# Performance work log

Measured on AMD Instinct MI355X. Metric: run time of the kernel, lower is better.

Reference implementation:

```python
import jax, jax.numpy as jnp
import numpy as np

N_HEADS = 4
D_K = 32
C = 128
SCALE = D_K ** (-0.5)


def setup_inputs() -> dict:
    key = jax.random.key(0)
    k1, k2, k3, k4, k5 = jax.random.split(key, 5)
    x = jax.random.normal(k1, (16, C, 32, 32), dtype=jnp.float32)
    # nn.Linear(C, n_heads*d_k*3): weight [out, in], bias [out]
    Wp = jax.random.normal(k2, (N_HEADS * D_K * 3, C), dtype=jnp.float32) * (C ** -0.5)
    bp = jax.random.normal(k3, (N_HEADS * D_K * 3,), dtype=jnp.float32) * 0.01
    # nn.Linear(n_heads*d_k, C)
    Wo = jax.random.normal(k4, (C, N_HEADS * D_K), dtype=jnp.float32) * ((N_HEADS * D_K) ** -0.5)
    bo = jax.random.normal(k5, (C,), dtype=jnp.float32) * 0.01
    return {"x": x, "Wp": Wp, "bp": bp, "Wo": Wo, "bo": bo}


def reference(x, Wp, bp, Wo, bo):
    b, c, h, w = x.shape
    n = h * w
    # (b,c,h,w) -> (b, n, c); NOTE: GroupNorm from __init__ is never applied in forward.
    xf = x.reshape(b, c, n).transpose(0, 2, 1)
    qkv = (xf @ Wp.T + bp).reshape(b, n, N_HEADS, 3 * D_K)
    q, k, v = jnp.split(qkv, 3, axis=-1)  # each (b, n, heads, d_k)
    attn = jnp.einsum('bihd,bjhd->bijh', q, k) * SCALE  # (b, n, n, heads)
    # Faithful to original: softmax over LAST axis = heads axis (original code bug)
    attn = jax.nn.softmax(attn, axis=-1)
    res = jnp.einsum('bijh,bjhd->bihd', attn, v).reshape(b, n, N_HEADS * D_K)
    res = res @ Wo.T + bo + xf
    return res.transpose(0, 2, 1).reshape(b, c, h, w)
```

## Files before the change

kernel.cpp:

```cpp
#include <hip/hip_runtime.h>

typedef short s8v __attribute__((ext_vector_type(8)));
typedef float f4v __attribute__((ext_vector_type(4)));

#define NTOK 1024
#define CD 128
#define QSCALE 0.25506953149031838f

__device__ __forceinline__ ushort f2bf(float x) {
    union { float f; unsigned u; } v; v.f = x;
    unsigned u = v.u + 0x7fff + ((v.u >> 16) & 1);
    return (ushort)(u >> 16);
}
__device__ __forceinline__ float bf2f(ushort x) {
    union { unsigned u; float f; } v; v.u = ((unsigned)x) << 16;
    return v.f;
}
__device__ __forceinline__ void gl_lds16(const ushort* g, ushort* l) {
    __builtin_amdgcn_global_load_lds(
        (const __attribute__((address_space(1))) unsigned int*)(g),
        (__attribute__((address_space(3))) unsigned int*)(l), 16, 0, 0);
}
__device__ __forceinline__ unsigned cvt_pk_bf16(float lo, float hi) {
    unsigned r;
    asm("v_cvt_pk_bf16_f32 %0, %1, %2" : "=v"(r) : "v"(lo), "v"(hi));
    return r;
}

__global__ __launch_bounds__(256) void k_pre(const float* __restrict__ x,
                                             const float* __restrict__ Wp,
                                             const float* __restrict__ Wo,
                                             ushort* __restrict__ xt,
                                             ushort* __restrict__ wpre) {
    const int t = threadIdx.x;
    const int bx = blockIdx.x;
    if (bx < 256) {
        __shared__ ushort tile[128 * 68];
        const int b = bx >> 4;
        const int n0 = (bx & 15) << 6;
        #pragma unroll
        for (int p = 0; p < 8; ++p) {
            const int c = p * 16 + (t >> 4);
            const int n4 = t & 15;
            const float4 v = *(const float4*)&x[(b * CD + c) * NTOK + n0 + n4 * 4];
            ushort4 o;
            o.x = f2bf(v.x); o.y = f2bf(v.y); o.z = f2bf(v.z); o.w = f2bf(v.w);
            *(ushort4*)&tile[c * 68 + n4 * 4] = o;
        }
        __syncthreads();
        #pragma unroll
        for (int p = 0; p < 4; ++p) {
            const int nl = t >> 2;
            const int g = (t & 3) + p * 4;
            s8v tmp;
            #pragma unroll
            for (int e = 0; e < 8; ++e) tmp[e] = (short)tile[(g * 8 + e) * 68 + nl];
            const int n = n0 + nl;
            *(s8v*)&xt[(b * NTOK + n) * CD + ((g ^ (nl & 7)) * 8)] = tmp;
        }
    } else {
        const int kind = bx - 256;
        ushort* dst = wpre + kind * (CD * CD);
        for (int e = t * 4; e < CD * CD; e += 1024) {
            const int f = e >> 7, c = e & 127;
            const float* src;
            if (kind == 3) src = &Wo[f * CD + c];
            else           src = &Wp[((f >> 5) * 96 + kind * 32 + (f & 31)) * CD + c];
            const float4 v = *(const float4*)src;
            ushort4 o;
            o.x = f2bf(v.x); o.y = f2bf(v.y); o.z = f2bf(v.z); o.w = f2bf(v.w);
            *(ushort4*)&dst[f * CD + (((c >> 3) ^ (f & 7)) * 8) + (c & 7)] = o;
        }
    }
}

__global__ __launch_bounds__(256) void k_proj(const ushort* __restrict__ xt,
                                              const ushort* __restrict__ wpre,
                                              const float* __restrict__ bp,
                                              ushort* __restrict__ qb,
                                              ushort* __restrict__ kb,
                                              ushort* __restrict__ vtb) {
    __shared__ ushort Abuf[128 * 128];
    __shared__ ushort Bbuf[64 * 128];
    const int t = threadIdx.x;
    const int lane = t & 63;
    const int w = t >> 6;
    const int li = lane & 15;
    const int lg = lane >> 4;
    const int bx = blockIdx.x;
    const int kind = bx >> 8;
    const int idx = bx & 255;

    const ushort* Asrc;
    const ushort* Bsrc;
    if (kind < 2) {
        Asrc = xt + (idx >> 1) * 128 * CD;
        Bsrc = wpre + kind * (CD * CD) + (idx & 1) * 64 * CD;
    } else {
        Asrc = wpre + 2 * (CD * CD);
        Bsrc = xt + idx * 64 * CD;
    }
    {
        const ushort* ga = Asrc + w * 4096;
        ushort* la = Abuf + w * 4096;
        #pragma unroll
        for (int i = 0; i < 8; ++i) gl_lds16(ga + i * 512 + lane * 8, la + i * 512);
        const ushort* gb = Bsrc + w * 2048;
        ushort* lb = Bbuf + w * 2048;
        #pragma unroll
        for (int i = 0; i < 4; ++i) gl_lds16(gb + i * 512 + lane * 8, lb + i * 512);
    }
    __syncthreads();

    const f4v fz = {0.f, 0.f, 0.f, 0.f};
    f4v acc[2][4];
    #pragma unroll
    for (int mf = 0; mf < 2; ++mf)
        #pragma unroll
        for (int nf = 0; nf < 4; ++nf) acc[mf][nf] = fz;
    const int m_base = w * 32;
    #pragma unroll
    for (int kk = 0; kk < 4; ++kk) {
        s8v a[2], bb[4];
        #pragma unroll
        for (int mf = 0; mf < 2; ++mf) {
            const int row = m_base + mf * 16 + li;
            a[mf] = *(const s8v*)&Abuf[row * CD + (((kk * 4 + lg) ^ (row & 7)) * 8)];
        }
        #pragma unroll
        for (int nf = 0; nf < 4; ++nf) {
            const int row = nf * 16 + li;
            bb[nf] = *(const s8v*)&Bbuf[row * CD + (((kk * 4 + lg) ^ (row & 7)) * 8)];
        }
        #pragma unroll
        for (int mf = 0; mf < 2; ++mf)
            #pragma unroll
            for (int nf = 0; nf < 4; ++nf)
                acc[mf][nf] = __builtin_amdgcn_mfma_f32_16x16x32_bf16(a[mf], bb[nf], acc[mf][nf], 0, 0, 0);
    }

    if (kind < 2) {
        ushort* dst = (kind == 0) ? qb : kb;
        const int m0 = (idx >> 1) * 128;
        const int f0 = (idx & 1) * 64;
        #pragma unroll
        for (int mf = 0; mf < 2; ++mf)
            #pragma unroll
            for (int nf = 0; nf < 4; ++nf) {
                const int f = f0 + nf * 16 + li;
                const int o = (f >> 5) * 96 + kind * 32 + (f & 31);
                const float bias = bp[o];
                #pragma unroll
                for (int r = 0; r < 4; ++r) {
                    const int row = m0 + m_base + mf * 16 + lg * 4 + r;
                    float v = acc[mf][nf][r] + bias;
                    if (kind == 0) v *= QSCALE;
                    dst[row * CD + f] = f2bf(v);
                }
            }
    } else {
        const int n0g = idx * 64;
        const int b = n0g >> 10;
        const int nl0 = n0g & 1023;
        #pragma unroll
        for (int mf = 0; mf < 2; ++mf)
            #pragma unroll
            for (int r = 0; r < 4; ++r) {
                const int f = m_base + mf * 16 + lg * 4 + r;
                const int o = (f >> 5) * 96 + 64 + (f & 31);
                const float bias = bp[o];
                #pragma unroll
                for (int nf = 0; nf < 4; ++nf) {
                    const int n = nl0 + nf * 16 + li;
                    const int jl = n & 31;
                    const int np = (n & ~31) | (((jl & 15) >> 2) * 8 + (jl & 3) + ((jl >> 4) << 2));
                    vtb[(b * CD + f) * NTOK + np] = f2bf(acc[mf][nf][r] + bias);
                }
            }
    }
}

__global__ __launch_bounds__(256) void k_attn(const ushort* __restrict__ qb,
                                              const ushort* __restrict__ kb,
                                              const ushort* __restrict__ vtb,
                                              ushort* __restrict__ res4) {
    __shared__ ushort kbuf[2][32 * 136];
    __shared__ ushort vbuf[3][128 * 40];
    const int t = threadIdx.x;
    const int lane = t & 63;
    const int w = t >> 6;
    const int b = blockIdx.x;
    const int it = blockIdx.y;
    const int js = blockIdx.z;
    const int i0 = it * 64 + w * 16;
    const int li = lane & 15;
    const int lg = lane >> 4;

    s8v qf[4];
    #pragma unroll
    for (int h = 0; h < 4; ++h)
        qf[h] = *(const s8v*)&qb[(b*NTOK + i0 + li)*CD + h*32 + lg*8];

    const f4v fz = {0.f, 0.f, 0.f, 0.f};
    f4v acc[4][2];
    #pragma unroll
    for (int h = 0; h < 4; ++h) { acc[h][0] = fz; acc[h][1] = fz; }

    const int j0 = js * 256;
    const ushort* kptr0 = &kb[(b*NTOK + j0 + (t>>4))*CD + (t&15)*8];
    const ushort* kptr1 = kptr0 + 16*CD;
    const ushort* vptr0 = &vtb[(b*CD + (t>>2))*NTOK + j0 + (t&3)*8];
    const ushort* vptr1 = vptr0 + 64*NTOK;
    const int kwo = (t>>4)*136 + (t&15)*8;
    const int vwo = (t>>2)*40 + (t&3)*8;

    s8v k0 = *(const s8v*)kptr0;
    s8v k1 = *(const s8v*)kptr1;
    s8v v0 = *(const s8v*)vptr0;
    s8v v1 = *(const s8v*)vptr1;
    *(s8v*)&kbuf[0][kwo]          = k0;
    *(s8v*)&kbuf[0][kwo + 16*136] = k1;
    *(s8v*)&vbuf[0][vwo]          = v0;
    *(s8v*)&vbuf[0][vwo + 64*40]  = v1;
    k0 = *(const s8v*)(kptr0 + 32*CD);
    k1 = *(const s8v*)(kptr1 + 32*CD);
    v0 = *(const s8v*)(vptr0 + 32);
    v1 = *(const s8v*)(vptr1 + 32);
    __syncthreads();

    unsigned wv[4][4];
    {
        f4v sv[4][2];
        __builtin_amdgcn_s_setprio(1);
        #pragma unroll
        for (int h = 0; h < 4; ++h)
            #pragma unroll
            for (int jh = 0; jh < 2; ++jh) {
                s8v kf = *(const s8v*)&kbuf[0][(jh*16 + li)*136 + h*32 + lg*8];
                sv[h][jh] = __builtin_amdgcn_mfma_f32_16x16x32_bf16(kf, qf[h], fz, 0, 0, 0);
            }
        __builtin_amdgcn_s_setprio(0);
        #pragma unroll
        for (int jh = 0; jh < 2; ++jh)
            #pragma unroll
            for (int r = 0; r < 4; ++r) {
                float e0 = __builtin_amdgcn_exp2f(sv[0][jh][r]);
                float e1 = __builtin_amdgcn_exp2f(sv[1][jh][r]);
                float e2 = __builtin_amdgcn_exp2f(sv[2][jh][r]);
                float e3 = __builtin_amdgcn_exp2f(sv[3][jh][r]);
                float inv = __builtin_amdgcn_rcpf(e0 + e1 + e2 + e3);
                sv[0][jh][r] = e0 * inv;
                sv[1][jh][r] = e1 * inv;
                sv[2][jh][r] = e2 * inv;
                sv[3][jh][r] = e3 * inv;
            }
        #pragma unroll
        for (int h = 0; h < 4; ++h) {
            wv[h][0] = cvt_pk_bf16(sv[h][0][0], sv[h][0][1]);
            wv[h][1] = cvt_pk_bf16(sv[h][0][2], sv[h][0][3]);
            wv[h][2] = cvt_pk_bf16(sv[h][1][0], sv[h][1][1]);
            wv[h][3] = cvt_pk_bf16(sv[h][1][2], sv[h][1][3]);
        }
    }

    #pragma unroll
    for (int tt = 1; tt <= 8; ++tt) {
        if (tt <= 7) {
            ushort* kn = kbuf[tt & 1];
            ushort* vn = vbuf[tt % 3];
            *(s8v*)&kn[kwo]          = k0;
            *(s8v*)&kn[kwo + 16*136] = k1;
            *(s8v*)&vn[vwo]          = v0;
            *(s8v*)&vn[vwo + 64*40]  = v1;
        }
        __syncthreads();
        if (tt <= 6) {
            k0 = *(const s8v*)(kptr0 + (tt+1)*32*CD);
            k1 = *(const s8v*)(kptr1 + (tt+1)*32*CD);
            v0 = *(const s8v*)(vptr0 + (tt+1)*32);
            v1 = *(const s8v*)(vptr1 + (tt+1)*32);
        }
        f4v sv[4][2];
        if (tt <= 7) {
            const ushort* kc = kbuf[tt & 1];
            __builtin_amdgcn_s_setprio(1);
            #pragma unroll
            for (int h = 0; h < 4; ++h)
                #pragma unroll
                for (int jh = 0; jh < 2; ++jh) {
                    s8v kf = *(const s8v*)&kc[(jh*16 + li)*136 + h*32 + lg*8];
                    sv[h][jh] = __builtin_amdgcn_mfma_f32_16x16x32_bf16(kf, qf[h], fz, 0, 0, 0);
                }
            __builtin_amdgcn_s_setprio(0);
        }
        {
            const ushort* vc = vbuf[(tt - 1) % 3];
            #pragma unroll
            for (int h = 0; h < 4; ++h) {
                union { unsigned d[4]; s8v s; } av;
                av.d[0] = wv[h][0]; av.d[1] = wv[h][1];
                av.d[2] = wv[h][2]; av.d[3] = wv[h][3];
                s8v vf0 = *(const s8v*)&vc[(h*32 + li)*40 + lg*8];
                s8v vf1 = *(const s8v*)&vc[(h*32 + 16 + li)*40 + lg*8];
                __builtin_amdgcn_s_setprio(1);
                acc[h][0] = __builtin_amdgcn_mfma_f32_16x16x32_bf16(av.s, vf0, acc[h][0], 0, 0, 0);
                acc[h][1] = __builtin_amdgcn_mfma_f32_16x16x32_bf16(av.s, vf1, acc[h][1], 0, 0, 0);
                __builtin_amdgcn_s_setprio(0);
            }
        }
        if (tt <= 7) {
            #pragma unroll
            for (int jh = 0; jh < 2; ++jh)
                #pragma unroll
                for (int r = 0; r < 4; ++r) {
                    float e0 = __builtin_amdgcn_exp2f(sv[0][jh][r]);
                    float e1 = __builtin_amdgcn_exp2f(sv[1][jh][r]);
                    float e2 = __builtin_amdgcn_exp2f(sv[2][jh][r]);
                    float e3 = __builtin_amdgcn_exp2f(sv[3][jh][r]);
                    float inv = __builtin_amdgcn_rcpf(e0 + e1 + e2 + e3);
                    sv[0][jh][r] = e0 * inv;
                    sv[1][jh][r] = e1 * inv;
                    sv[2][jh][r] = e2 * inv;
                    sv[3][jh][r] = e3 * inv;
                }
            #pragma unroll
            for (int h = 0; h < 4; ++h) {
                wv[h][0] = cvt_pk_bf16(sv[h][0][0], sv[h][0][1]);
                wv[h][1] = cvt_pk_bf16(sv[h][0][2], sv[h][0][3]);
                wv[h][2] = cvt_pk_bf16(sv[h][1][0], sv[h][1][1]);
                wv[h][3] = cvt_pk_bf16(sv[h][1][2], sv[h][1][3]);
            }
        }
    }

    #pragma unroll
    for (int h = 0; h < 4; ++h)
        #pragma unroll
        for (int dh = 0; dh < 2; ++dh)
            #pragma unroll
            for (int r = 0; r < 4; ++r) {
                const int i = i0 + lg*4 + r;
                const int f = h*32 + dh*16 + li;
                res4[js*(16*NTOK*CD) + (b*NTOK + i)*CD + f] = f2bf(acc[h][dh][r]);
            }
}

__global__ __launch_bounds__(256) void k_out(const ushort* __restrict__ wpre,
                                             const ushort* __restrict__ res4,
                                             const float* __restrict__ bo,
                                             const float* __restrict__ x,
                                             float* __restrict__ out) {
    __shared__ ushort Abuf[128 * 128];
    __shared__ ushort Bbuf[64 * 128];
    const int t = threadIdx.x;
    const int lane = t & 63;
    const int w = t >> 6;
    const int li = lane & 15;
    const int lg = lane >> 4;
    const int idx = blockIdx.x;
    const int n0g = idx * 64;
    const int b = n0g >> 10;
    {
        const ushort* ga = wpre + 3 * (CD * CD) + w * 4096;
        ushort* la = Abuf + w * 4096;
        #pragma unroll
        for (int i = 0; i < 8; ++i) gl_lds16(ga + i * 512 + lane * 8, la + i * 512);
    }
    for (int u = t; u < 64 * 16; u += 256) {
        const int rl = u >> 4, g = u & 15;
        const ushort* p = &res4[(n0g + rl) * CD + g * 8];
        s8v p0 = *(const s8v*)(p);
        s8v p1 = *(const s8v*)(p + 16*NTOK*CD);
        s8v p2 = *(const s8v*)(p + 32*NTOK*CD);
        s8v p3 = *(const s8v*)(p + 48*NTOK*CD);
        s8v sm;
        #pragma unroll
        for (int e = 0; e < 8; ++e)
            sm[e] = (short)f2bf(bf2f((ushort)p0[e]) + bf2f((ushort)p1[e])
                              + bf2f((ushort)p2[e]) + bf2f((ushort)p3[e]));
        *(s8v*)&Bbuf[rl * CD + ((g ^ (rl & 7)) * 8)] = sm;
    }
    __syncthreads();

    const f4v fz = {0.f, 0.f, 0.f, 0.f};
    f4v acc[2][4];
    #pragma unroll
    for (int mf = 0; mf < 2; ++mf)
        #pragma unroll
        for (int nf = 0; nf < 4; ++nf) acc[mf][nf] = fz;
    const int m_base = w * 32;
    #pragma unroll
    for (int kk = 0; kk < 4; ++kk) {
        s8v a[2], bb[4];
        #pragma unroll
        for (int mf = 0; mf < 2; ++mf) {
            const int row = m_base + mf * 16 + li;
            a[mf] = *(const s8v*)&Abuf[row * CD + (((kk * 4 + lg) ^ (row & 7)) * 8)];
        }
        #pragma unroll
        for (int nf = 0; nf < 4; ++nf) {
            const int row = nf * 16 + li;
            bb[nf] = *(const s8v*)&Bbuf[row * CD + (((kk * 4 + lg) ^ (row & 7)) * 8)];
        }
        #pragma unroll
        for (int mf = 0; mf < 2; ++mf)
            #pragma unroll
            for (int nf = 0; nf < 4; ++nf)
                acc[mf][nf] = __builtin_amdgcn_mfma_f32_16x16x32_bf16(a[mf], bb[nf], acc[mf][nf], 0, 0, 0);
    }
    const int nl0 = n0g & 1023;
    #pragma unroll
    for (int mf = 0; mf < 2; ++mf)
        #pragma unroll
        for (int r = 0; r < 4; ++r) {
            const int o = m_base + mf * 16 + lg * 4 + r;
            const float bias = bo[o];
            #pragma unroll
            for (int nf = 0; nf < 4; ++nf) {
                const int n = nl0 + nf * 16 + li;
                const int gi = (b * CD + o) * NTOK + n;
                out[gi] = acc[mf][nf][r] + bias + x[gi];
            }
        }
}

extern "C" void kernel_launch(void* const* d_in, const int* in_sizes, int n_in,
                              void* d_out, int out_size, void* d_ws, size_t ws_size,
                              hipStream_t stream) {
    const float* x  = (const float*)d_in[0];
    const float* Wp = (const float*)d_in[1];
    const float* bp = (const float*)d_in[2];
    const float* Wo = (const float*)d_in[3];
    const float* bo = (const float*)d_in[4];
    float* out = (float*)d_out;
    ushort* xt   = (ushort*)d_ws;
    ushort* wpre = xt + 16*1024*128;
    ushort* qbw  = wpre + 4*128*128;
    ushort* kbw  = qbw + 16*1024*128;
    ushort* vtb  = kbw + 16*1024*128;
    ushort* res4 = vtb + 16*1024*128;
    k_pre <<<260, 256, 0, stream>>>(x, Wp, Wo, xt, wpre);
    k_proj<<<768, 256, 0, stream>>>(xt, wpre, bp, qbw, kbw, vtb);
    k_attn<<<dim3(16, 16, 4), 256, 0, stream>>>(qbw, kbw, vtb, res4);
    k_out <<<256, 256, 0, stream>>>(wpre, res4, bo, x, out);
}
```

Baseline: 49.52 us.

## Load V fragments directly from global into registers, drop V LDS staging

Removes the triple-buffered LDS staging of the transposed V tile. Each lane now loads its MFMA B-operand fragments straight from global memory into registers and prefetches the next tile after the PV MFMAs. This saves LDS writes, LDS reads and shared memory, which may raise occupancy. In exchange each wave issues redundant, less-coalesced global loads (16-byte chunks strided by NTOK), and the prefetch distance is shorter, so global latency may be exposed.

```diff
diff --git a/kernel.cpp b/kernel.cpp
--- a/kernel.cpp
+++ b/kernel.cpp
@@ -185,7 +185,6 @@
                                               const ushort* __restrict__ vtb,
                                               ushort* __restrict__ res4) {
     __shared__ ushort kbuf[2][32 * 136];
-    __shared__ ushort vbuf[3][128 * 40];
     const int t = threadIdx.x;
     const int lane = t & 63;
     const int w = t >> 6;
@@ -209,23 +208,21 @@
     const int j0 = js * 256;
     const ushort* kptr0 = &kb[(b*NTOK + j0 + (t>>4))*CD + (t&15)*8];
     const ushort* kptr1 = kptr0 + 16*CD;
-    const ushort* vptr0 = &vtb[(b*CD + (t>>2))*NTOK + j0 + (t&3)*8];
-    const ushort* vptr1 = vptr0 + 64*NTOK;
     const int kwo = (t>>4)*136 + (t&15)*8;
-    const int vwo = (t>>2)*40 + (t&3)*8;
+    const ushort* vfb = &vtb[(b*CD + li)*NTOK + j0 + lg*8];
 
     s8v k0 = *(const s8v*)kptr0;
     s8v k1 = *(const s8v*)kptr1;
-    s8v v0 = *(const s8v*)vptr0;
-    s8v v1 = *(const s8v*)vptr1;
     *(s8v*)&kbuf[0][kwo]          = k0;
     *(s8v*)&kbuf[0][kwo + 16*136] = k1;
-    *(s8v*)&vbuf[0][vwo]          = v0;
-    *(s8v*)&vbuf[0][vwo + 64*40]  = v1;
+    s8v vf[4][2];
+    #pragma unroll
+    for (int h = 0; h < 4; ++h)
+        #pragma unroll
+        for (int dh = 0; dh < 2; ++dh)
+            vf[h][dh] = *(const s8v*)&vfb[(h*32 + dh*16)*NTOK];
     k0 = *(const s8v*)(kptr0 + 32*CD);
     k1 = *(const s8v*)(kptr1 + 32*CD);
-    v0 = *(const s8v*)(vptr0 + 32);
-    v1 = *(const s8v*)(vptr1 + 32);
     __syncthreads();
 
     unsigned wv[4][4];
@@ -267,18 +264,13 @@
     for (int tt = 1; tt <= 8; ++tt) {
         if (tt <= 7) {
             ushort* kn = kbuf[tt & 1];
-            ushort* vn = vbuf[tt % 3];
             *(s8v*)&kn[kwo]          = k0;
             *(s8v*)&kn[kwo + 16*136] = k1;
-            *(s8v*)&vn[vwo]          = v0;
-            *(s8v*)&vn[vwo + 64*40]  = v1;
         }
         __syncthreads();
         if (tt <= 6) {
             k0 = *(const s8v*)(kptr0 + (tt+1)*32*CD);
             k1 = *(const s8v*)(kptr1 + (tt+1)*32*CD);
-            v0 = *(const s8v*)(vptr0 + (tt+1)*32);
-            v1 = *(const s8v*)(vptr1 + (tt+1)*32);
         }
         f4v sv[4][2];
         if (tt <= 7) {
@@ -293,20 +285,22 @@
                 }
             __builtin_amdgcn_s_setprio(0);
         }
-        {
-            const ushort* vc = vbuf[(tt - 1) % 3];
-            #pragma unroll
-            for (int h = 0; h < 4; ++h) {
-                union { unsigned d[4]; s8v s; } av;
-                av.d[0] = wv[h][0]; av.d[1] = wv[h][1];
-                av.d[2] = wv[h][2]; av.d[3] = wv[h][3];
-                s8v vf0 = *(const s8v*)&vc[(h*32 + li)*40 + lg*8];
-                s8v vf1 = *(const s8v*)&vc[(h*32 + 16 + li)*40 + lg*8];
-                __builtin_amdgcn_s_setprio(1);
-                acc[h][0] = __builtin_amdgcn_mfma_f32_16x16x32_bf16(av.s, vf0, acc[h][0], 0, 0, 0);
-                acc[h][1] = __builtin_amdgcn_mfma_f32_16x16x32_bf16(av.s, vf1, acc[h][1], 0, 0, 0);
-                __builtin_amdgcn_s_setprio(0);
-            }
+        #pragma unroll
+        for (int h = 0; h < 4; ++h) {
+            union { unsigned d[4]; s8v s; } av;
+            av.d[0] = wv[h][0]; av.d[1] = wv[h][1];
+            av.d[2] = wv[h][2]; av.d[3] = wv[h][3];
+            __builtin_amdgcn_s_setprio(1);
+            acc[h][0] = __builtin_amdgcn_mfma_f32_16x16x32_bf16(av.s, vf[h][0], acc[h][0], 0, 0, 0);
+            acc[h][1] = __builtin_amdgcn_mfma_f32_16x16x32_bf16(av.s, vf[h][1], acc[h][1], 0, 0, 0);
+            __builtin_amdgcn_s_setprio(0);
+        }
+        if (tt <= 7) {
+            #pragma unroll
+            for (int h = 0; h < 4; ++h)
+                #pragma unroll
+                for (int dh = 0; dh < 2; ++dh)
+                    vf[h][dh] = *(const s8v*)&vfb[(h*32 + dh*16)*NTOK + tt*32];
         }
         if (tt <= 7) {
             #pragma unroll
```

Measured after the change: 63.80 us. +28.8%, slower.
